# Kernel optimization log

Measured on AMD Instinct MI355X. Metric: run time of the kernel, lower is better.

The kernel has to match this reference:

```python
import jax, jax.numpy as jnp
import numpy as np

N_NODES = 20000


def _gcn_norm(edge_index, n):
    src, dst = edge_index[0], edge_index[1]
    # degree of A + I (self-loops), all edge weights 1
    deg = jax.ops.segment_sum(jnp.ones(src.shape[0], jnp.float32), dst, num_segments=n) + 1.0
    dinv = jax.lax.rsqrt(deg)
    norm = dinv[src] * dinv[dst]          # [E]
    self_norm = dinv * dinv               # [N] self-loop coefficient = 1/deg
    return src, dst, norm, self_norm


def _gcn_layer(x, W, b, src, dst, norm, self_norm):
    # x: [B, N, Fin]; W: [Fin, Fout]
    h = jnp.einsum('bnf,fo->bno', x, W)   # transform first (PyG GCNConv order)
    msg = h[:, src, :] * norm[None, :, None]                      # [B, E, Fout]
    agg = jax.vmap(lambda m: jax.ops.segment_sum(m, dst, num_segments=x.shape[1]))(msg)
    agg = agg + h * self_norm[None, :, None]                      # self-loop term
    return agg + b


def setup_inputs() -> dict:
    key = jax.random.key(0)
    ks = jax.random.split(key, 8)
    B, N, Fin, H, O, E = 2, N_NODES, 256, 256, 64, 320000
    s = lambda f: 1.0 / np.sqrt(f)
    return {
        'x': jax.random.normal(ks[0], (B, N, Fin), jnp.float32),
        'W1': jax.random.normal(ks[1], (Fin, H), jnp.float32) * s(Fin),
        'b1': jnp.zeros((H,), jnp.float32),
        'W2': jax.random.normal(ks[2], (H, H), jnp.float32) * s(H),
        'b2': jnp.zeros((H,), jnp.float32),
        'Wfc': jax.random.normal(ks[3], (H, O), jnp.float32) * s(H),
        'bfc': jnp.zeros((O,), jnp.float32),
        'edge_index': jax.random.randint(ks[4], (2, E), 0, N, jnp.int64),
    }


def reference(x, W1, b1, W2, b2, Wfc, bfc, edge_index):
    src, dst, norm, self_norm = _gcn_norm(edge_index, x.shape[1])
    h = jax.nn.relu(_gcn_layer(x, W1, b1, src, dst, norm, self_norm))
    h = jax.nn.relu(_gcn_layer(h, W2, b2, src, dst, norm, self_norm))
    pooled = jnp.mean(h, axis=1)          # mean over nodes -> [B, H]
    return pooled @ Wfc + bfc             # [B, O]
```

## Files before the change

kernel.cpp:

```cpp
#include <hip/hip_runtime.h>

#define NNODES 20000
#define BATCH  2
#define FEAT   256
#define OOUT   64
#define PBLK   200
#define MROWS  40000
#define NPB    20096
#define H8ROWS 40192

typedef short  bhalf8 __attribute__((ext_vector_type(8)));
typedef float  floatx4 __attribute__((ext_vector_type(4)));
typedef float  floatx2 __attribute__((ext_vector_type(2)));

__device__ __forceinline__ float bf2f(unsigned short u) {
  return __uint_as_float(((unsigned int)u) << 16);
}
__device__ __forceinline__ unsigned short f2bf(float f) {
  unsigned int u = __float_as_uint(f);
  return (unsigned short)((u + 0x7fffu + ((u >> 16) & 1u)) >> 16);
}
__device__ __forceinline__ unsigned int pack4_fp8(float a, float b, float c, float d) {
  int p = __builtin_amdgcn_cvt_pk_fp8_f32(a, b, 0, false);
  p = __builtin_amdgcn_cvt_pk_fp8_f32(c, d, p, true);
  return (unsigned int)p;
}

__global__ __launch_bounds__(256) void prep_kernel(const float* __restrict__ W1,
                                                   const float* __restrict__ W2,
                                                   unsigned short* __restrict__ w1hi,
                                                   unsigned short* __restrict__ w1lo,
                                                   unsigned short* __restrict__ w2hi,
                                                   unsigned short* __restrict__ w2lo,
                                                   const int* __restrict__ raw, int E,
                                                   int* __restrict__ flag,
                                                   int* __restrict__ cnt,
                                                   int* __restrict__ fill) {
  int bid = blockIdx.x, tid = threadIdx.x;
  int idx = bid * 256 + tid;
  int which = idx >> 16, loc = idx & 65535;
  const float* W = which ? W2 : W1;
  unsigned short* Whi = which ? w2hi : w1hi;
  unsigned short* Wlo = which ? w2lo : w1lo;
  int k = loc >> 8, n = loc & 255;
  float w = W[loc];
  unsigned short hi = f2bf(w);
  unsigned short lo = f2bf(w - bf2f(hi));
  int g = n >> 4, ln = n & 15;
  int ks = k >> 5, ch = (k >> 3) & 3, j = k & 7;
  int addr = ((ks * 16 + g) * 64 + ch * 16 + ln) * 8 + j;
  Whi[addr] = hi;
  Wlo[addr] = lo;
  if (idx < NNODES) { cnt[idx] = 0; fill[idx] = 0; }
  if (bid == 511) {
    __shared__ int any;
    if (tid == 0) any = 0;
    __syncthreads();
    int nchk = E < 2048 ? E : 2048;
    for (int i = tid; i < nchk; i += 256)
      if (raw[2 * i + 1] != 0) any = 1;
    __syncthreads();
    if (tid == 0) *flag = any;
  }
}

__global__ void convert_count_kernel(const int* __restrict__ raw, const int* __restrict__ flag,
                                     int* __restrict__ s32, int* __restrict__ d32,
                                     int* __restrict__ cnt, int E) {
  int e = blockIdx.x * blockDim.x + threadIdx.x;
  if (e >= E) return;
  int s, d;
  if (*flag) { s = raw[e];     d = raw[E + e]; }
  else       { s = raw[2 * e]; d = raw[2 * (E + e)]; }
  s32[e] = s; d32[e] = d;
  atomicAdd(&cnt[d], 1);
}

__global__ __launch_bounds__(1024) void scan_dinv_kernel(const int* __restrict__ cnt,
                                                         int* __restrict__ row_start,
                                                         float* __restrict__ dinv, int n) {
  __shared__ int wsum[16];
  __shared__ int carry_s;
  int tid = threadIdx.x, lane = tid & 63, wv = tid >> 6;
  if (tid == 0) carry_s = 0;
  __syncthreads();
  for (int base = 0; base < n; base += 1024) {
    int v = (base + tid < n) ? cnt[base + tid] : 0;
    if (base + tid < n) dinv[base + tid] = 1.0f / sqrtf((float)(v + 1));
    int x = v;
#pragma unroll
    for (int off = 1; off < 64; off <<= 1) {
      int t = __shfl_up(x, off);
      if (lane >= off) x += t;
    }
    if (lane == 63) wsum[wv] = x;
    __syncthreads();
    int carry = carry_s;
    if (wv == 0) {
      int s = (lane < 16) ? wsum[lane] : 0;
#pragma unroll
      for (int off = 1; off < 16; off <<= 1) {
        int t = __shfl_up(s, off);
        if (lane >= off) s += t;
      }
      if (lane < 16) wsum[lane] = s;
    }
    __syncthreads();
    int woff = wv ? wsum[wv - 1] : 0;
    int total = wsum[15];
    if (base + tid < n) row_start[base + tid] = carry + woff + x - v;
    __syncthreads();
    if (tid == 0) carry_s = carry + total;
  }
  if (tid == 0) row_start[n] = carry_s;
}

__global__ void scatter_kernel(const int* __restrict__ s32, const int* __restrict__ d32,
                               const int* __restrict__ row_start, int* __restrict__ fill,
                               const float* __restrict__ dinv,
                               int* __restrict__ csr_src, float* __restrict__ csr_norm, int E) {
  int e = blockIdx.x * blockDim.x + threadIdx.x;
  if (e >= E) return;
  int s = s32[e], d = d32[e];
  int p = row_start[d] + atomicAdd(&fill[d], 1);
  csr_src[p] = s;
  csr_norm[p] = dinv[s] * dinv[d];
}

template <int AFP32>
__global__ __launch_bounds__(256) void gemm_mfma(const void* __restrict__ Av,
                                                 const unsigned short* __restrict__ Whi,
                                                 const unsigned short* __restrict__ Wlo,
                                                 unsigned int* __restrict__ C) {
  __shared__ unsigned short lds[2][8192];
  int bid = blockIdx.x;
  int tile = bid >> 1, half = bid & 1;
  int b = tile >= 157 ? 1 : 0;
  int nbase = (tile - b * 157) * 128;
  int tid = threadIdx.x, lane = tid & 63, wv = tid >> 6;
  int kc = (lane >> 4) * 8;

  const float* Af          = (const float*)Av;
  const unsigned short* Ab = (const unsigned short*)Av;

  int nn[2], mr[2];
#pragma unroll
  for (int t = 0; t < 2; ++t) {
    int nl = nbase + wv * 32 + t * 16 + (lane & 15);
    nn[t] = nl;
    int ncl = nl > NNODES - 1 ? NNODES - 1 : nl;
    mr[t] = b * NNODES + ncl;
  }

  floatx4 acc[2][8];
#pragma unroll
  for (int t = 0; t < 2; ++t)
#pragma unroll
    for (int g = 0; g < 8; ++g) acc[t][g] = (floatx4)(0.0f);

  bhalf8 st[4];
  auto stage_load = [&](int ks) {
#pragma unroll
    for (int i2 = 0; i2 < 4; ++i2) {
      int u = i2 * 256 + tid;
      int hl = u >> 9, g = (u >> 6) & 7, l = u & 63;
      const unsigned short* Wp = hl ? Wlo : Whi;
      st[i2] = *(const bhalf8*)&Wp[((size_t)(ks * 16 + half * 8 + g) * 64 + l) * 8];
    }
  };
  auto stage_write = [&](int buf) {
#pragma unroll
    for (int i2 = 0; i2 < 4; ++i2) {
      int u = i2 * 256 + tid;
      *(bhalf8*)&lds[buf][(size_t)u * 8] = st[i2];
    }
  };
  auto load_a = [&](int ks, bhalf8 (&a)[2]) {
#pragma unroll
    for (int t = 0; t < 2; ++t) {
      if (AFP32) {
        const float* p = &Af[(size_t)mr[t] * FEAT + ks * 32 + kc];
        float4 u = *(const float4*)p;
        float4 v = *(const float4*)(p + 4);
        a[t][0] = (short)f2bf(u.x); a[t][1] = (short)f2bf(u.y);
        a[t][2] = (short)f2bf(u.z); a[t][3] = (short)f2bf(u.w);
        a[t][4] = (short)f2bf(v.x); a[t][5] = (short)f2bf(v.y);
        a[t][6] = (short)f2bf(v.z); a[t][7] = (short)f2bf(v.w);
      } else {
        a[t] = *(const bhalf8*)&Ab[(size_t)mr[t] * FEAT + ks * 32 + kc];
      }
    }
  };
  auto step = [&](int buf, bhalf8 (&a)[2]) {
#pragma unroll
    for (int g = 0; g < 8; ++g) {
      bhalf8 bh = *(const bhalf8*)&lds[buf][((size_t)g * 64 + lane) * 8];
      bhalf8 bl = *(const bhalf8*)&lds[buf][((size_t)(512 + g * 64) + lane) * 8];
#pragma unroll
      for (int t = 0; t < 2; ++t)
        acc[t][g] = __builtin_amdgcn_mfma_f32_16x16x32_bf16(bh, a[t], acc[t][g], 0, 0, 0);
#pragma unroll
      for (int t = 0; t < 2; ++t)
        acc[t][g] = __builtin_amdgcn_mfma_f32_16x16x32_bf16(bl, a[t], acc[t][g], 0, 0, 0);
    }
  };

  stage_load(0);
  stage_write(0);
  __syncthreads();
  bhalf8 aC[2];
  load_a(0, aC);
  int cur = 0;
#pragma unroll
  for (int ks = 0; ks < 8; ++ks) {
    bhalf8 aN[2];
    if (ks < 7) {
      stage_load(ks + 1);
      load_a(ks + 1, aN);
    }
    step(cur, aC);
    if (ks < 7) {
      stage_write(cur ^ 1);
      __syncthreads();
      aC[0] = aN[0]; aC[1] = aN[1];
    }
    cur ^= 1;
  }

  int nc = (lane >> 4) * 4;
#pragma unroll
  for (int t = 0; t < 2; ++t) {
    size_t r = (size_t)nn[t] * 2 + b;
#pragma unroll
    for (int g = 0; g < 8; ++g) {
      int col = (half * 8 + g) * 16 + nc;
      C[r * 64 + (col >> 2)] =
          pack4_fp8(acc[t][g][0], acc[t][g][1], acc[t][g][2], acc[t][g][3]);
    }
  }
}

__global__ __launch_bounds__(128) void agg_kernel(const uint4* __restrict__ h8,
                                                  const int* __restrict__ row_start,
                                                  const int* __restrict__ csr_src,
                                                  const float* __restrict__ csr_norm,
                                                  const float* __restrict__ dinv,
                                                  const float* __restrict__ bias,
                                                  unsigned short* __restrict__ out) {
  int n = blockIdx.x;
  int tid = threadIdx.x;
  int wave = tid >> 6, lane = tid & 63;
  int q = (wave << 1) | (lane >> 5);
  int cl = lane & 31;

  float a[16];
#pragma unroll
  for (int j = 0; j < 16; ++j) a[j] = 0.0f;

  auto dec_fma = [&](uint4 m, float w) {
    unsigned int mm[4] = {m.x, m.y, m.z, m.w};
#pragma unroll
    for (int j = 0; j < 4; ++j) {
      floatx2 lo = __builtin_amdgcn_cvt_pk_f32_fp8((int)mm[j], false);
      floatx2 hi = __builtin_amdgcn_cvt_pk_f32_fp8((int)mm[j], true);
      a[j * 4 + 0] = fmaf(w, lo[0], a[j * 4 + 0]);
      a[j * 4 + 1] = fmaf(w, lo[1], a[j * 4 + 1]);
      a[j * 4 + 2] = fmaf(w, hi[0], a[j * 4 + 2]);
      a[j * 4 + 3] = fmaf(w, hi[1], a[j * 4 + 3]);
    }
  };

  float di = dinv[n];
  if (q == 0) dec_fma(h8[(size_t)n * 32 + cl], di * di);

  int s0 = row_start[n], s1 = row_start[n + 1];
  int i = s0 + q;
  for (; i + 4 < s1; i += 8) {
    int sa = csr_src[i], sb = csr_src[i + 4];
    float wa = csr_norm[i], wb = csr_norm[i + 4];
    uint4 ma = h8[(size_t)sa * 32 + cl];
    uint4 mb = h8[(size_t)sb * 32 + cl];
    dec_fma(ma, wa);
    dec_fma(mb, wb);
  }
  if (i < s1) dec_fma(h8[(size_t)csr_src[i] * 32 + cl], csr_norm[i]);

#pragma unroll
  for (int j = 0; j < 16; ++j) a[j] += __shfl_xor(a[j], 32);

  __shared__ float red[32][17];
  if (wave == 1 && lane < 32) {
#pragma unroll
    for (int j = 0; j < 16; ++j) red[lane][j] = a[j];
  }
  __syncthreads();
  if (wave == 0 && lane < 32) {
    int b = cl >> 4;
    int c = (cl & 15) * 16;
#pragma unroll
    for (int j = 0; j < 16; ++j) a[j] += red[lane][j];
    unsigned short o[16];
#pragma unroll
    for (int j = 0; j < 16; ++j)
      o[j] = f2bf(fmaxf(a[j] + bias[c + j], 0.0f));
    unsigned short* dst = &out[((size_t)b * NNODES + n) * FEAT + c];
    *(uint4*)dst = *(uint4*)&o[0];
    *(uint4*)(dst + 8) = *(uint4*)&o[8];
  }
}

__global__ __launch_bounds__(256) void pool_partial(const unsigned short* __restrict__ h2,
                                                    float* __restrict__ partials) {
  int blk = blockIdx.x;
  int c = threadIdx.x;
  int chunk = NNODES / PBLK;
  int n0 = blk * chunk;
  float s0 = 0.f, s1 = 0.f;
  for (int n = n0; n < n0 + chunk; ++n) {
    s0 += bf2f(h2[((size_t)0 * NNODES + n) * FEAT + c]);
    s1 += bf2f(h2[((size_t)1 * NNODES + n) * FEAT + c]);
  }
  partials[(blk * 2 + 0) * FEAT + c] = s0;
  partials[(blk * 2 + 1) * FEAT + c] = s1;
}

__global__ __launch_bounds__(256) void pool_fc(const float* __restrict__ partials,
                                               const float* __restrict__ Wfc, const float* __restrict__ bfc,
                                               float* __restrict__ out) {
  __shared__ float pooled[BATCH][FEAT];
  int t = threadIdx.x;
  float s0 = 0.f, s1 = 0.f;
  for (int p = 0; p < PBLK; ++p) {
    s0 += partials[(p * 2 + 0) * FEAT + t];
    s1 += partials[(p * 2 + 1) * FEAT + t];
  }
  pooled[0][t] = s0 / (float)NNODES;
  pooled[1][t] = s1 / (float)NNODES;
  __syncthreads();
  if (t < BATCH * OOUT) {
    int b = t >> 6, o = t & 63;
    float acc = bfc[o];
    for (int c2 = 0; c2 < FEAT; ++c2)
      acc = fmaf(pooled[b][c2], Wfc[c2 * OOUT + o], acc);
    out[b * OOUT + o] = acc;
  }
}

extern "C" void kernel_launch(void* const* d_in, const int* in_sizes, int n_in,
                              void* d_out, int out_size, void* d_ws, size_t ws_size,
                              hipStream_t stream) {
  const float* x    = (const float*)d_in[0];
  const float* W1   = (const float*)d_in[1];
  const float* b1   = (const float*)d_in[2];
  const float* W2   = (const float*)d_in[3];
  const float* b2   = (const float*)d_in[4];
  const float* Wfc  = (const float*)d_in[5];
  const float* bfc  = (const float*)d_in[6];
  const int*   eraw = (const int*)d_in[7];
  int E = in_sizes[7] / 2;
  float* out = (float*)d_out;

  char* ws = (char*)d_ws;
  size_t off = 0;
  auto alloc = [&](size_t elems4B) -> void* {
    void* p = ws + off * 4;
    off += (elems4B + 3) & ~(size_t)3;
    return p;
  };
  int*   flag      = (int*)alloc(4);
  int*   s32       = (int*)alloc(E);
  int*   d32       = (int*)alloc(E);
  int*   cnt       = (int*)alloc(NNODES);
  float* dinv      = (float*)alloc(NNODES);
  int*   row_start = (int*)alloc(NNODES + 1);
  int*   fill      = (int*)alloc(NNODES);
  int*   csr_src   = (int*)alloc(E);
  float* csr_norm  = (float*)alloc(E);
  unsigned short* w1hi = (unsigned short*)alloc(65536 / 2);
  unsigned short* w1lo = (unsigned short*)alloc(65536 / 2);
  unsigned short* w2hi = (unsigned short*)alloc(65536 / 2);
  unsigned short* w2lo = (unsigned short*)alloc(65536 / 2);
  unsigned int*   h8   = (unsigned int*)alloc((size_t)H8ROWS * 64);
  unsigned short* a1   = (unsigned short*)alloc((size_t)MROWS * FEAT / 2);
  float* partials  = (float*)alloc((size_t)PBLK * BATCH * FEAT);

  int eg = (E + 255) / 256;
  prep_kernel<<<512, 256, 0, stream>>>(W1, W2, w1hi, w1lo, w2hi, w2lo, eraw, E, flag, cnt, fill);
  convert_count_kernel<<<eg, 256, 0, stream>>>(eraw, flag, s32, d32, cnt, E);
  scan_dinv_kernel<<<1, 1024, 0, stream>>>(cnt, row_start, dinv, NNODES);
  scatter_kernel<<<eg, 256, 0, stream>>>(s32, d32, row_start, fill, dinv, csr_src, csr_norm, E);

  gemm_mfma<1><<<628, 256, 0, stream>>>(x, w1hi, w1lo, h8);
  agg_kernel<<<NNODES, 128, 0, stream>>>((const uint4*)h8, row_start, csr_src, csr_norm, dinv, b1, a1);
  gemm_mfma<0><<<628, 256, 0, stream>>>(a1, w2hi, w2lo, h8);
  agg_kernel<<<NNODES, 128, 0, stream>>>((const uint4*)h8, row_start, csr_src, csr_norm, dinv, b2, a1);
  pool_partial<<<PBLK, 256, 0, stream>>>(a1, partials);
  pool_fc<<<1, 256, 0, stream>>>(partials, Wfc, bfc, out);
}
```

Baseline: 188.9 us.

## Parallelize CSR prefix scan across chunks, drop edge copies, remap GEMM tiles

Replaces the single-block prefix scan over node degrees with a 20-block chunked scan whose per-chunk offsets are accumulated atomically and added when row pointers are read. Removes the intermediate int32 src/dst arrays so the scatter re-reads raw edge indices. Also remaps GEMM block indices so that groups of 8 tiles run for one weight half before switching, padding the grid to 640 blocks with early exits. Adds an extra indirection on row pointers in the aggregation kernel.

```diff
diff --git a/kernel.cpp b/kernel.cpp
--- a/kernel.cpp
+++ b/kernel.cpp
@@ -8,6 +8,7 @@
 #define MROWS  40000
 #define NPB    20096
 #define H8ROWS 40192
+#define NCHUNK 20
 
 typedef short  bhalf8 __attribute__((ext_vector_type(8)));
 typedef float  floatx4 __attribute__((ext_vector_type(4)));
@@ -35,7 +36,8 @@
                                                    const int* __restrict__ raw, int E,
                                                    int* __restrict__ flag,
                                                    int* __restrict__ cnt,
-                                                   int* __restrict__ fill) {
+                                                   int* __restrict__ fill,
+                                                   int* __restrict__ chunkOff) {
   int bid = blockIdx.x, tid = threadIdx.x;
   int idx = bid * 256 + tid;
   int which = idx >> 16, loc = idx & 65535;
@@ -52,6 +54,7 @@
   Whi[addr] = hi;
   Wlo[addr] = lo;
   if (idx < NNODES) { cnt[idx] = 0; fill[idx] = 0; }
+  if (idx < NCHUNK) chunkOff[idx] = 0;
   if (bid == 511) {
     __shared__ int any;
     if (tid == 0) any = 0;
@@ -64,65 +67,61 @@
   }
 }
 
-__global__ void convert_count_kernel(const int* __restrict__ raw, const int* __restrict__ flag,
-                                     int* __restrict__ s32, int* __restrict__ d32,
-                                     int* __restrict__ cnt, int E) {
+__global__ void count_kernel(const int* __restrict__ raw, const int* __restrict__ flag,
+                             int* __restrict__ cnt, int E) {
+  int e = blockIdx.x * blockDim.x + threadIdx.x;
+  if (e >= E) return;
+  int d = (*flag) ? raw[E + e] : raw[2 * (E + e)];
+  atomicAdd(&cnt[d], 1);
+}
+
+__global__ __launch_bounds__(256) void scan_a_kernel(const int* __restrict__ cnt,
+                                                     int* __restrict__ row_start,
+                                                     float* __restrict__ dinv,
+                                                     int* __restrict__ chunkOff) {
+  int c = blockIdx.x, tid = threadIdx.x;
+  int base = c * 1024 + tid * 4;
+  int v[4]; int tsum = 0;
+#pragma unroll
+  for (int j = 0; j < 4; ++j) {
+    v[j] = (base + j < NNODES) ? cnt[base + j] : 0;
+    tsum += v[j];
+  }
+  int lane = tid & 63, wv = tid >> 6;
+  int x = tsum;
+#pragma unroll
+  for (int off = 1; off < 64; off <<= 1) {
+    int t = __shfl_up(x, off);
+    if (lane >= off) x += t;
+  }
+  __shared__ int wsum[4];
+  if (lane == 63) wsum[wv] = x;
+  __syncthreads();
+  int woff = 0;
+  for (int w = 0; w < wv; ++w) woff += wsum[w];
+  int run = woff + x - tsum;
+#pragma unroll
+  for (int j = 0; j < 4; ++j) {
+    if (base + j <= NNODES) row_start[base + j] = run;
+    if (base + j < NNODES) dinv[base + j] = 1.0f / sqrtf((float)(v[j] + 1));
+    run += v[j];
+  }
+  if (tid == 0) {
+    int T = wsum[0] + wsum[1] + wsum[2] + wsum[3];
+    for (int c2 = c + 1; c2 < NCHUNK; ++c2) atomicAdd(&chunkOff[c2], T);
+  }
+}
+
+__global__ void scatter_kernel(const int* __restrict__ raw, const int* __restrict__ flag,
+                               const int* __restrict__ row_start, const int* __restrict__ chunkOff,
+                               int* __restrict__ fill, const float* __restrict__ dinv,
+                               int* __restrict__ csr_src, float* __restrict__ csr_norm, int E) {
   int e = blockIdx.x * blockDim.x + threadIdx.x;
   if (e >= E) return;
   int s, d;
   if (*flag) { s = raw[e];     d = raw[E + e]; }
   else       { s = raw[2 * e]; d = raw[2 * (E + e)]; }
-  s32[e] = s; d32[e] = d;
-  atomicAdd(&cnt[d], 1);
-}
-
-__global__ __launch_bounds__(1024) void scan_dinv_kernel(const int* __restrict__ cnt,
-                                                         int* __restrict__ row_start,
-                                                         float* __restrict__ dinv, int n) {
-  __shared__ int wsum[16];
-  __shared__ int carry_s;
-  int tid = threadIdx.x, lane = tid & 63, wv = tid >> 6;
-  if (tid == 0) carry_s = 0;
-  __syncthreads();
-  for (int base = 0; base < n; base += 1024) {
-    int v = (base + tid < n) ? cnt[base + tid] : 0;
-    if (base + tid < n) dinv[base + tid] = 1.0f / sqrtf((float)(v + 1));
-    int x = v;
-#pragma unroll
-    for (int off = 1; off < 64; off <<= 1) {
-      int t = __shfl_up(x, off);
-      if (lane >= off) x += t;
-    }
-    if (lane == 63) wsum[wv] = x;
-    __syncthreads();
-    int carry = carry_s;
-    if (wv == 0) {
-      int s = (lane < 16) ? wsum[lane] : 0;
-#pragma unroll
-      for (int off = 1; off < 16; off <<= 1) {
-        int t = __shfl_up(s, off);
-        if (lane >= off) s += t;
-      }
-      if (lane < 16) wsum[lane] = s;
-    }
-    __syncthreads();
-    int woff = wv ? wsum[wv - 1] : 0;
-    int total = wsum[15];
-    if (base + tid < n) row_start[base + tid] = carry + woff + x - v;
-    __syncthreads();
-    if (tid == 0) carry_s = carry + total;
-  }
-  if (tid == 0) row_start[n] = carry_s;
-}
-
-__global__ void scatter_kernel(const int* __restrict__ s32, const int* __restrict__ d32,
-                               const int* __restrict__ row_start, int* __restrict__ fill,
-                               const float* __restrict__ dinv,
-                               int* __restrict__ csr_src, float* __restrict__ csr_norm, int E) {
-  int e = blockIdx.x * blockDim.x + threadIdx.x;
-  if (e >= E) return;
-  int s = s32[e], d = d32[e];
-  int p = row_start[d] + atomicAdd(&fill[d], 1);
+  int p = row_start[d] + chunkOff[d >> 10] + atomicAdd(&fill[d], 1);
   csr_src[p] = s;
   csr_norm[p] = dinv[s] * dinv[d];
 }
@@ -132,9 +131,11 @@
                                                  const unsigned short* __restrict__ Whi,
                                                  const unsigned short* __restrict__ Wlo,
                                                  unsigned int* __restrict__ C) {
+  int bid = blockIdx.x;
+  int tile = (bid >> 4) * 8 + (bid & 7);
+  int half = (bid >> 3) & 1;
+  if (tile >= 314) return;
   __shared__ unsigned short lds[2][8192];
-  int bid = blockIdx.x;
-  int tile = bid >> 1, half = bid & 1;
   int b = tile >= 157 ? 1 : 0;
   int nbase = (tile - b * 157) * 128;
   int tid = threadIdx.x, lane = tid & 63, wv = tid >> 6;
@@ -242,6 +243,7 @@
 
 __global__ __launch_bounds__(128) void agg_kernel(const uint4* __restrict__ h8,
                                                   const int* __restrict__ row_start,
+                                                  const int* __restrict__ chunkOff,
                                                   const int* __restrict__ csr_src,
                                                   const float* __restrict__ csr_norm,
                                                   const float* __restrict__ dinv,
@@ -273,7 +275,8 @@
   float di = dinv[n];
   if (q == 0) dec_fma(h8[(size_t)n * 32 + cl], di * di);
 
-  int s0 = row_start[n], s1 = row_start[n + 1];
+  int s0 = row_start[n] + chunkOff[n >> 10];
+  int s1 = row_start[n + 1] + chunkOff[(n + 1) >> 10];
   int i = s0 + q;
   for (; i + 4 < s1; i += 8) {
     int sa = csr_src[i], sb = csr_src[i + 4];
@@ -368,12 +371,11 @@
     return p;
   };
   int*   flag      = (int*)alloc(4);
-  int*   s32       = (int*)alloc(E);
-  int*   d32       = (int*)alloc(E);
   int*   cnt       = (int*)alloc(NNODES);
   float* dinv      = (float*)alloc(NNODES);
   int*   row_start = (int*)alloc(NNODES + 1);
   int*   fill      = (int*)alloc(NNODES);
+  int*   chunkOff  = (int*)alloc(NCHUNK + 4);
   int*   csr_src   = (int*)alloc(E);
   float* csr_norm  = (float*)alloc(E);
   unsigned short* w1hi = (unsigned short*)alloc(65536 / 2);
@@ -385,15 +387,19 @@
   float* partials  = (float*)alloc((size_t)PBLK * BATCH * FEAT);
 
   int eg = (E + 255) / 256;
-  prep_kernel<<<512, 256, 0, stream>>>(W1, W2, w1hi, w1lo, w2hi, w2lo, eraw, E, flag, cnt, fill);
-  convert_count_kernel<<<eg, 256, 0, stream>>>(eraw, flag, s32, d32, cnt, E);
-  scan_dinv_kernel<<<1, 1024, 0, stream>>>(cnt, row_start, dinv, NNODES);
-  scatter_kernel<<<eg, 256, 0, stream>>>(s32, d32, row_start, fill, dinv, csr_src, csr_norm, E);
-
-  gemm_mfma<1><<<628, 256, 0, stream>>>(x, w1hi, w1lo, h8);
-  agg_kernel<<<NNODES, 128, 0, stream>>>((const uint4*)h8, row_start, csr_src, csr_norm, dinv, b1, a1);
-  gemm_mfma<0><<<628, 256, 0, stream>>>(a1, w2hi, w2lo, h8);
-  agg_kernel<<<NNODES, 128, 0, stream>>>((const uint4*)h8, row_start, csr_src, csr_norm, dinv, b2, a1);
+  prep_kernel<<<512, 256, 0, stream>>>(W1, W2, w1hi, w1lo, w2hi, w2lo, eraw, E, flag,
+                                       cnt, fill, chunkOff);
+  count_kernel<<<eg, 256, 0, stream>>>(eraw, flag, cnt, E);
+  scan_a_kernel<<<NCHUNK, 256, 0, stream>>>(cnt, row_start, dinv, chunkOff);
+  scatter_kernel<<<eg, 256, 0, stream>>>(eraw, flag, row_start, chunkOff, fill, dinv,
+                                         csr_src, csr_norm, E);
+
+  gemm_mfma<1><<<640, 256, 0, stream>>>(x, w1hi, w1lo, h8);
+  agg_kernel<<<NNODES, 128, 0, stream>>>((const uint4*)h8, row_start, chunkOff,
+                                         csr_src, csr_norm, dinv, b1, a1);
+  gemm_mfma<0><<<640, 256, 0, stream>>>(a1, w2hi, w2lo, h8);
+  agg_kernel<<<NNODES, 128, 0, stream>>>((const uint4*)h8, row_start, chunkOff,
+                                         csr_src, csr_norm, dinv, b2, a1);
   pool_partial<<<PBLK, 256, 0, stream>>>(a1, partials);
   pool_fc<<<1, 256, 0, stream>>>(partials, Wfc, bfc, out);
 }
```

New measurement: 177.9 us. 5.8% less time.
